# Kernel tuning notes

Hardware: AMD Instinct MI355X
Metric: run time of the kernel (lower is better)

Reference implementation:

```python
import jax, jax.numpy as jnp
import numpy as np
from functools import partial

IMG = 800.0
LEVEL_HW = [13, 25, 50, 100, 200]  # p6..p2 (reverse-sorted dict order)
NUM_A = 3
A_TOTAL = NUM_A * sum(h * h for h in LEVEL_HW)  # 159882


def _rand_boxes(key, shape, img=IMG):
    k1, k2, k3, k4 = jax.random.split(key, 4)
    cx = jax.random.uniform(k1, shape, minval=0.0, maxval=img)
    cy = jax.random.uniform(k2, shape, minval=0.0, maxval=img)
    w = jax.random.uniform(k3, shape, minval=16.0, maxval=256.0)
    h = jax.random.uniform(k4, shape, minval=16.0, maxval=256.0)
    return jnp.stack([cx - w / 2, cy - h / 2, cx + w / 2, cy + h / 2], axis=-1)


def setup_inputs() -> dict:
    key = jax.random.key(0)
    ks = jax.random.split(key, 16)
    feats = {}
    for i, (name, hw) in enumerate(zip(['f_p6', 'f_p5', 'f_p4', 'f_p3', 'f_p2'], LEVEL_HW)):
        feats[name] = jax.random.normal(ks[i], (2, 256, hw, hw), dtype=jnp.float32)
    anchors = _rand_boxes(ks[5], (A_TOTAL,))
    gt_bboxes = _rand_boxes(ks[6], (2, 20))
    w_in = jax.random.normal(ks[7], (256, 256, 3, 3), dtype=jnp.float32) * 0.02
    b_in = jnp.zeros((256,), jnp.float32)
    w_obj = jax.random.normal(ks[8], (3, 256, 1, 1), dtype=jnp.float32) * 0.02
    b_obj = jnp.zeros((3,), jnp.float32)
    w_del = jax.random.normal(ks[9], (12, 256, 1, 1), dtype=jnp.float32) * 0.02
    b_del = jnp.zeros((12,), jnp.float32)
    return dict(**feats, anchors=anchors, gt_bboxes=gt_bboxes,
                w_in=w_in, b_in=b_in, w_obj=w_obj, b_obj=b_obj,
                w_del=w_del, b_del=b_del)


def _conv(x, w, b, pad):
    y = jax.lax.conv_general_dilated(x, w, (1, 1), [(pad, pad), (pad, pad)],
                                     dimension_numbers=('NCHW', 'OIHW', 'NCHW'))
    return y + b[None, :, None, None]


def _pairwise_iou(b1, b2):
    # b1 [A,4], b2 [G,4] -> [A,G]
    a1 = (b1[:, 2] - b1[:, 0]) * (b1[:, 3] - b1[:, 1])
    a2 = (b2[:, 2] - b2[:, 0]) * (b2[:, 3] - b2[:, 1])
    lt = jnp.maximum(b1[:, None, :2], b2[None, :, :2])
    rb = jnp.minimum(b1[:, None, 2:], b2[None, :, 2:])
    wh = jnp.clip(rb - lt, 0.0)
    inter = wh[..., 0] * wh[..., 1]
    return inter / (a1[:, None] + a2[None, :] - inter)


def _get_deltas(src, tgt):
    sw = src[:, 2] - src[:, 0]; sh = src[:, 3] - src[:, 1]
    scx = src[:, 0] + 0.5 * sw; scy = src[:, 1] + 0.5 * sh
    tw = tgt[:, 2] - tgt[:, 0]; th = tgt[:, 3] - tgt[:, 1]
    tcx = tgt[:, 0] + 0.5 * tw; tcy = tgt[:, 1] + 0.5 * th
    return jnp.stack([(tcx - scx) / sw, (tcy - scy) / sh,
                      jnp.log(tw / sw), jnp.log(th / sh)], axis=-1)


def _per_image(logits, deltas, gt, anchors):
    # logits [A], deltas [A,4], gt [G,4]
    iou = _pairwise_iou(anchors, gt)                      # [A,G]
    matched = jnp.argmax(iou, axis=1)                     # [A]
    mval = jnp.max(iou, axis=1)
    label = jnp.where(mval >= 0.7, 1.0, jnp.where(mval < 0.3, 0.0, -1.0))
    # low-quality matches: best anchor per gt is positive
    best_per_gt = jnp.max(iou, axis=0)                    # [G]
    lq = jnp.any((iou == best_per_gt[None, :]) & (best_per_gt[None, :] > 0), axis=1)
    label = jnp.where(lq, 1.0, label)
    # deterministic subsample: up to 128 pos, fill to 256 with neg
    pos_mask = label == 1.0
    neg_mask = label == 0.0
    sel_pos = pos_mask & (jnp.cumsum(pos_mask.astype(jnp.int32)) <= 128)
    n_pos = jnp.sum(sel_pos.astype(jnp.int32))
    sel_neg = neg_mask & (jnp.cumsum(neg_mask.astype(jnp.int32)) <= (256 - n_pos))
    valid = sel_pos | sel_neg
    # BCE with logits, sum over sampled anchors
    tgt = jnp.clip(label, 0.0, 1.0)
    bce = jnp.maximum(logits, 0.0) - logits * tgt + jnp.log1p(jnp.exp(-jnp.abs(logits)))
    obj_loss = jnp.sum(jnp.where(valid, bce, 0.0))
    # smooth-L1 with beta=0 == L1, only on positives
    gt_d = _get_deltas(anchors, gt[matched])              # [A,4]
    l1 = jnp.sum(jnp.abs(deltas - gt_d), axis=-1)
    loc_loss = jnp.sum(jnp.where(sel_pos, l1, 0.0))
    return obj_loss, loc_loss


def _forward(f_p6, f_p5, f_p4, f_p3, f_p2, anchors, gt_bboxes,
             w_in, b_in, w_obj, b_obj, w_del, b_del):
    logits_all, deltas_all = [], []
    for fm in (f_p6, f_p5, f_p4, f_p3, f_p2):  # reverse-sorted fm order
        x = jax.nn.relu(_conv(fm, w_in, b_in, 1))
        lg = _conv(x, w_obj, b_obj, 0)                    # [B,3,H,W]
        dl = _conv(x, w_del, b_del, 0)                    # [B,12,H,W]
        B, _, H, W = lg.shape
        logits_all.append(jnp.transpose(lg, (0, 2, 3, 1)).reshape(B, -1))
        dl = dl.reshape(B, NUM_A, 4, H, W)
        deltas_all.append(jnp.transpose(dl, (0, 3, 4, 1, 2)).reshape(B, -1, 4))
    logits = jnp.concatenate(logits_all, axis=1)          # [B,A]
    deltas = jnp.concatenate(deltas_all, axis=1)          # [B,A,4]
    obj, loc = jax.vmap(_per_image, in_axes=(0, 0, 0, None))(logits, deltas, gt_bboxes, anchors)
    return (obj[0] + obj[1]) / 2.0, (loc[0] + loc[1]) / 2.0


def reference(f_p6, f_p5, f_p4, f_p3, f_p2, anchors, gt_bboxes,
              w_in, b_in, w_obj, b_obj, w_del, b_del):
    return _forward(f_p6, f_p5, f_p4, f_p3, f_p2, anchors, gt_bboxes,
                    w_in, b_in, w_obj, b_obj, w_del, b_del)
```

## Files before the change

kernel.cpp:

```cpp
#include <hip/hip_runtime.h>
#include <hip/hip_bf16.h>
#include <math.h>

#define A_TOTAL 159882
#define NGT 20
#define NBLK 625
#define ANB 4
#define WTBLK 288


__device__ __forceinline__ float iou_one(float ax1, float ay1, float ax2, float ay2,
                                         float gx1, float gy1, float gx2, float gy2) {
    float a1 = (ax2 - ax1) * (ay2 - ay1);
    float a2 = (gx2 - gx1) * (gy2 - gy1);
    float ltx = fmaxf(ax1, gx1), lty = fmaxf(ay1, gy1);
    float rbx = fminf(ax2, gx2), rby = fminf(ay2, gy2);
    float w = fmaxf(rbx - ltx, 0.f), h = fmaxf(rby - lty, 0.f);
    float inter = w * h;
    return inter / (a1 + a2 - inter);
}

__device__ __forceinline__ void decode_anchor(int a, int& W, int& aid, int& y, int& x, int& lvl) {
    int off;
    if      (a < 507)   { off = 0;     W = 13;  lvl = 0; }
    else if (a < 2382)  { off = 507;   W = 25;  lvl = 1; }
    else if (a < 9882)  { off = 2382;  W = 50;  lvl = 2; }
    else if (a < 39882) { off = 9882;  W = 100; lvl = 3; }
    else                { off = 39882; W = 200; lvl = 4; }
    int rel = a - off;
    aid = rel % 3;
    int pos = rel / 3;
    y = pos / W; x = pos % W;
}

__global__ __launch_bounds__(256) void k1_bmax_wtrans(
    const float* __restrict__ anchors, const float* __restrict__ gt,
    const float* __restrict__ w_in,
    float* __restrict__ pmax, float* __restrict__ wt) {
    const int bx = blockIdx.x, img = blockIdx.y;
    const int tid = threadIdx.x;
    if (bx >= NBLK) {
        int idx = ((bx - NBLK) * 2 + img) * 256 + tid;
        int co = idx / 576, k4 = idx - co * 576;
        float4 v = *(const float4*)(w_in + (size_t)co * 2304 + k4 * 4);
        ((float4*)wt)[(size_t)k4 * 256 + co] = v;
        return;
    }
    __shared__ float sgt[NGT * 4];
    __shared__ float sred[4][NGT];
    if (tid < NGT * 4) sgt[tid] = gt[img * NGT * 4 + tid];
    __syncthreads();
    const int a = bx * 256 + tid;
    float4 ab = make_float4(0.f, 0.f, 1.f, 1.f);
    if (a < A_TOTAL) ab = ((const float4*)anchors)[a];
    const int lane = tid & 63, wid = tid >> 6;
    #pragma unroll
    for (int g = 0; g < NGT; g++) {
        float u = (a < A_TOTAL)
                    ? iou_one(ab.x, ab.y, ab.z, ab.w,
                              sgt[g * 4], sgt[g * 4 + 1], sgt[g * 4 + 2], sgt[g * 4 + 3])
                    : 0.f;
        #pragma unroll
        for (int o = 32; o > 0; o >>= 1) u = fmaxf(u, __shfl_down(u, o));
        if (lane == 0) sred[wid][g] = u;
    }
    __syncthreads();
    if (tid < NGT) {
        float u = fmaxf(fmaxf(sred[0][tid], sred[1][tid]),
                        fmaxf(sred[2][tid], sred[3][tid]));
        pmax[((size_t)img * NBLK + bx) * NGT + tid] = u;
    }
}

__global__ __launch_bounds__(256) void k2_label(
    const float* __restrict__ anchors, const float* __restrict__ gt,
    const float* __restrict__ pmax,
    unsigned char* __restrict__ packed, unsigned int* __restrict__ blk_cnt) {
    const int img = blockIdx.y, blk = blockIdx.x;
    const int tid = threadIdx.x;
    const int lane = tid & 63, wid = tid >> 6;
    __shared__ float sgt[NGT * 4];
    __shared__ float sred[4][NGT];
    __shared__ float bestl[NGT];
    __shared__ int wp[4], wn[4];
    if (tid < NGT * 4) sgt[tid] = gt[img * NGT * 4 + tid];

    float bl[NGT];
    #pragma unroll
    for (int g = 0; g < NGT; g++) bl[g] = 0.f;
    for (int i = tid; i < NBLK; i += 256) {
        const float* pr = pmax + ((size_t)img * NBLK + i) * NGT;
        #pragma unroll
        for (int g = 0; g < NGT; g++) bl[g] = fmaxf(bl[g], pr[g]);
    }
    #pragma unroll
    for (int g = 0; g < NGT; g++) {
        float u = bl[g];
        #pragma unroll
        for (int o = 32; o > 0; o >>= 1) u = fmaxf(u, __shfl_down(u, o));
        if (lane == 0) sred[wid][g] = u;
    }
    __syncthreads();
    if (tid < NGT)
        bestl[tid] = fmaxf(fmaxf(sred[0][tid], sred[1][tid]),
                           fmaxf(sred[2][tid], sred[3][tid]));
    __syncthreads();

    const int a = blk * 256 + tid;
    const bool act = a < A_TOTAL;
    int code = 2;
    if (act) {
        float4 ab = ((const float4*)anchors)[a];
        float mval = -1.f; int arg = 0; bool lq = false;
        #pragma unroll
        for (int g = 0; g < NGT; g++) {
            float v = iou_one(ab.x, ab.y, ab.z, ab.w,
                              sgt[g * 4], sgt[g * 4 + 1], sgt[g * 4 + 2], sgt[g * 4 + 3]);
            if (v > mval) { mval = v; arg = g; }
            if (__float_as_uint(v) == __float_as_uint(bestl[g]) && v > 0.f) lq = true;
        }
        if (lq || mval >= 0.7f) code = 1;
        else if (mval < 0.3f)   code = 0;
        packed[(size_t)img * A_TOTAL + a] = (unsigned char)((code << 5) | arg);
    }
    unsigned long long bp = __ballot(act && code == 1);
    unsigned long long bn = __ballot(act && code == 0);
    if (lane == 0) { wp[wid] = __popcll(bp); wn[wid] = __popcll(bn); }
    __syncthreads();
    if (tid == 0) {
        unsigned int p = wp[0] + wp[1] + wp[2] + wp[3];
        unsigned int n = wn[0] + wn[1] + wn[2] + wn[3];
        blk_cnt[img * NBLK + blk] = (p << 16) | n;
    }
}

__global__ __launch_bounds__(256) void k3_select(
    const unsigned char* __restrict__ packed,
    const unsigned int* __restrict__ blk_cnt,
    int* __restrict__ sel, int* __restrict__ sel_count) {
    const int img = blockIdx.y, blk = blockIdx.x;
    const int tid = threadIdx.x;
    const int lane = tid & 63, wid = tid >> 6;
    __shared__ unsigned long long sscan[8];
    __shared__ int wcnt[8];

    unsigned long long tot = 0ULL, pre = 0ULL;
    const int j0 = tid * 3;
    #pragma unroll
    for (int j = 0; j < 3; j++) {
        int i = j0 + j;
        if (i < NBLK) {
            unsigned u = blk_cnt[img * NBLK + i];
            unsigned long long w = ((unsigned long long)(u >> 16) << 32) | (u & 0xFFFFu);
            tot += w;
            if (i < blk) pre += w;
        }
    }
    #pragma unroll
    for (int o = 32; o > 0; o >>= 1) {
        tot += __shfl_down(tot, o);
        pre += __shfl_down(pre, o);
    }
    if (lane == 0) { sscan[wid] = tot; sscan[4 + wid] = pre; }
    __syncthreads();
    unsigned long long tota = sscan[0] + sscan[1] + sscan[2] + sscan[3];
    unsigned long long prea = sscan[4] + sscan[5] + sscan[6] + sscan[7];
    int tp = (int)(tota >> 32), tn = (int)(tota & 0xFFFFFFFFull);
    int npos = min(tp, 128), capn = 256 - npos;
    if (blk == 0 && tid == 0) sel_count[img] = npos + min(tn, capn);
    int base_p = (int)(prea >> 32), base_n = (int)(prea & 0xFFFFFFFFull);

    const int a = blk * 256 + tid;
    const bool act = a < A_TOTAL;
    int code = act ? (packed[(size_t)img * A_TOTAL + a] >> 5) : 2;
    const bool isp = act && code == 1;
    const bool isn = act && code == 0;
    unsigned long long bp = __ballot(isp);
    unsigned long long bn = __ballot(isn);
    if (lane == 0) { wcnt[wid] = __popcll(bp); wcnt[4 + wid] = __popcll(bn); }
    __syncthreads();
    const unsigned long long mlt = (1ULL << lane) - 1ULL;
    int rp = __popcll(bp & mlt), rn = __popcll(bn & mlt);
    for (int w = 0; w < 4; w++)
        if (w < wid) { rp += wcnt[w]; rn += wcnt[4 + w]; }
    if (isp) { int r = base_p + rp; if (r < npos) sel[img * 256 + r] = a | (1 << 30); }
    if (isn) { int r = base_n + rn; if (r < capn) sel[img * 256 + npos + r] = a; }
}

template <int TRM>
__device__ __forceinline__ void stage_patches(
    const float* __restrict__ f0, const float* __restrict__ f1,
    const float* __restrict__ f2, const float* __restrict__ f3,
    const float* __restrict__ f4,
    const int* __restrict__ sel, int nsel, int img, int chunk, int slot0,
    float (&patch)[ANB][TRM],
    int (&s_W)[ANB], int (&s_y)[ANB], int (&s_x)[ANB], int (&s_act)[ANB],
    const float* (&s_fm)[ANB]) {
    constexpr int CIP = TRM / 9;
    const int tid = threadIdx.x;
    if (tid < ANB) {
        int slot = slot0 + tid;
        bool act = slot < nsel;
        int e = act ? sel[img * 256 + slot] : 0;
        int a = e & 0x3FFFFFFF;
        int W, aid, y, x, lvl;
        decode_anchor(a, W, aid, y, x, lvl);
        s_W[tid] = W; s_y[tid] = y; s_x[tid] = x; s_act[tid] = act ? 1 : 0;
        s_fm[tid] = (lvl == 0 ? f0 : lvl == 1 ? f1 : lvl == 2 ? f2 : lvl == 3 ? f3 : f4);
    }
    __syncthreads();
    for (int p = tid; p < ANB * TRM; p += 256) {
        int aa = p / TRM;
        int idx = p - aa * TRM;
        int cil = idx / 9;
        int r = idx - cil * 9;
        int ky = r / 3, kx = r - ky * 3;
        int W = s_W[aa];
        int yy = s_y[aa] + ky - 1, xx = s_x[aa] + kx - 1;
        float v = 0.f;
        if (s_act[aa] && yy >= 0 && yy < W && xx >= 0 && xx < W) {
            const float* fm = s_fm[aa];
            int ci = chunk * CIP + cil;
            v = fm[(((size_t)img * 256 + ci) * W + yy) * W + xx];
        }
        patch[aa][idx] = v;
    }
    __syncthreads();
}

template <int NCH>
__global__ __launch_bounds__(256) void k_convT(
    const float* __restrict__ f0, const float* __restrict__ f1,
    const float* __restrict__ f2, const float* __restrict__ f3,
    const float* __restrict__ f4,
    const float* __restrict__ wt,
    const int* __restrict__ sel, const int* __restrict__ sel_count,
    float* __restrict__ xpart) {
    constexpr int CIP = 256 / NCH;
    constexpr int TRM = CIP * 9;
    const int img = blockIdx.z;
    const int chunk = blockIdx.y;
    const int slot0 = blockIdx.x * ANB;
    const int nsel = sel_count[img];
    if (slot0 >= nsel) return;

    __shared__ __align__(16) float patch[ANB][TRM];
    __shared__ int s_W[ANB], s_y[ANB], s_x[ANB], s_act[ANB];
    __shared__ const float* s_fm[ANB];
    stage_patches<TRM>(f0, f1, f2, f3, f4, sel, nsel, img, chunk, slot0,
                       patch, s_W, s_y, s_x, s_act, s_fm);

    const int c = threadIdx.x;
    const float4* wt4 = (const float4*)wt + (size_t)(chunk * (TRM / 4)) * 256 + c;
    const float4* p0 = (const float4*)patch[0];
    const float4* p1 = (const float4*)patch[1];
    const float4* p2 = (const float4*)patch[2];
    const float4* p3 = (const float4*)patch[3];
    float acc0 = 0.f, acc1 = 0.f, acc2 = 0.f, acc3 = 0.f;
    #pragma unroll 8
    for (int i = 0; i < TRM / 4; i++) {
        float4 w = wt4[(size_t)i * 256];
        float4 q;
        q = p0[i]; acc0 += w.x * q.x + w.y * q.y + w.z * q.z + w.w * q.w;
        q = p1[i]; acc1 += w.x * q.x + w.y * q.y + w.z * q.z + w.w * q.w;
        q = p2[i]; acc2 += w.x * q.x + w.y * q.y + w.z * q.z + w.w * q.w;
        q = p3[i]; acc3 += w.x * q.x + w.y * q.y + w.z * q.z + w.w * q.w;
    }
    float acc[ANB] = {acc0, acc1, acc2, acc3};
    #pragma unroll
    for (int aa = 0; aa < ANB; aa++) {
        int slot = slot0 + aa;
        if (slot < nsel)
            xpart[(((size_t)img * NCH + chunk) * 256 + slot) * 256 + c] = acc[aa];
    }
}

template <int NCH>
__global__ __launch_bounds__(256) void k_post(
    const float* __restrict__ xpart,
    const float* __restrict__ anchors, const float* __restrict__ gt,
    const float* __restrict__ b_in,
    const float* __restrict__ w_obj, const float* __restrict__ b_obj,
    const float* __restrict__ w_del, const float* __restrict__ b_del,
    const unsigned char* __restrict__ packed,
    const int* __restrict__ sel, const int* __restrict__ sel_count,
    float* __restrict__ lossbuf) {
    const int img = blockIdx.y;
    const int slot = blockIdx.x;
    const int nsel = sel_count[img];
    if (slot >= nsel) return;
    const int e = sel[img * 256 + slot];
    const int is_pos = (e >> 30) & 1;
    const int a = e & 0x3FFFFFFF;
    int W, aid, y, x, lvl;
    decode_anchor(a, W, aid, y, x, lvl);

    const int c = threadIdx.x;
    float s = b_in[c];
    #pragma unroll
    for (int ch = 0; ch < NCH; ch++)
        s += xpart[(((size_t)img * NCH + ch) * 256 + slot) * 256 + c];
    float xf = fmaxf(s, 0.f);

    float part[5];
    part[0] = xf * w_obj[aid * 256 + c];
    #pragma unroll
    for (int j = 0; j < 4; j++) part[1 + j] = xf * w_del[(aid * 4 + j) * 256 + c];
    const int lane = c & 63, wid = c >> 6;
    __shared__ float red[5][4];
    #pragma unroll
    for (int o = 32; o > 0; o >>= 1)
        #pragma unroll
        for (int j = 0; j < 5; j++) part[j] += __shfl_down(part[j], o);
    if (lane == 0)
        #pragma unroll
        for (int j = 0; j < 5; j++) red[j][wid] = part[j];
    __syncthreads();

    if (c == 0) {
        float logit = red[0][0] + red[0][1] + red[0][2] + red[0][3] + b_obj[aid];
        float tgt = is_pos ? 1.f : 0.f;
        float bce = fmaxf(logit, 0.f) - logit * tgt + log1pf(expf(-fabsf(logit)));
        float l1 = 0.f;
        if (is_pos) {
            float d[4];
            #pragma unroll
            for (int j = 0; j < 4; j++)
                d[j] = red[1 + j][0] + red[1 + j][1] + red[1 + j][2] + red[1 + j][3] + b_del[aid * 4 + j];
            int m = packed[(size_t)img * A_TOTAL + a] & 31;
            const float* sp = anchors + (size_t)a * 4;
            const float* t = gt + (size_t)(img * NGT + m) * 4;
            float sw = sp[2] - sp[0], sh = sp[3] - sp[1];
            float scx = sp[0] + 0.5f * sw, scy = sp[1] + 0.5f * sh;
            float tw = t[2] - t[0], th = t[3] - t[1];
            float tcx = t[0] + 0.5f * tw, tcy = t[1] + 0.5f * th;
            float g0 = (tcx - scx) / sw, g1 = (tcy - scy) / sh;
            float g2 = logf(tw / sw),    g3 = logf(th / sh);
            l1 = fabsf(d[0] - g0) + fabsf(d[1] - g1) + fabsf(d[2] - g2) + fabsf(d[3] - g3);
        }
        lossbuf[(img * 256 + slot) * 2 + 0] = bce;
        lossbuf[(img * 256 + slot) * 2 + 1] = l1;
    }
}

__global__ void k_final(const float* __restrict__ lossbuf,
                        const int* __restrict__ sel_count,
                        float* __restrict__ out) {
    const int t = threadIdx.x;
    const int img = t >> 8, slot = t & 255;
    float bce = 0.f, l1 = 0.f;
    if (slot < sel_count[img]) {
        bce = lossbuf[t * 2 + 0];
        l1  = lossbuf[t * 2 + 1];
    }
    const int lane = t & 63, wid = t >> 6;
    #pragma unroll
    for (int o = 32; o > 0; o >>= 1) {
        bce += __shfl_down(bce, o);
        l1  += __shfl_down(l1, o);
    }
    __shared__ float rb[8], rl[8];
    if (lane == 0) { rb[wid] = bce; rl[wid] = l1; }
    __syncthreads();
    if (t == 0) {
        float sb = 0.f, sl = 0.f;
        #pragma unroll
        for (int w = 0; w < 8; w++) { sb += rb[w]; sl += rl[w]; }
        out[0] = 0.5f * sb;
        out[1] = 0.5f * sl;
    }
}

__global__ void k_init(unsigned int* best, float* out) {
    int t = threadIdx.x;
    if (t < 2 * NGT) best[t] = 0u;
    if (t < 2) out[t] = 0.f;
}

__global__ void k_best(const float* __restrict__ anchors, const float* __restrict__ gt,
                       unsigned int* best) {
    const int img = blockIdx.y;
    __shared__ float sgt[NGT * 4];
    __shared__ float sred[4][NGT];
    const int tid = threadIdx.x;
    if (tid < NGT * 4) sgt[tid] = gt[img * NGT * 4 + tid];
    __syncthreads();
    float vmax[NGT];
    #pragma unroll
    for (int g = 0; g < NGT; g++) vmax[g] = 0.f;
    const int stride = gridDim.x * blockDim.x;
    for (int a = blockIdx.x * blockDim.x + tid; a < A_TOTAL; a += stride) {
        float4 ab = ((const float4*)anchors)[a];
        #pragma unroll
        for (int g = 0; g < NGT; g++) {
            float v = iou_one(ab.x, ab.y, ab.z, ab.w,
                              sgt[g * 4], sgt[g * 4 + 1], sgt[g * 4 + 2], sgt[g * 4 + 3]);
            vmax[g] = fmaxf(vmax[g], v);
        }
    }
    const int lane = tid & 63, wid = tid >> 6;
    #pragma unroll
    for (int g = 0; g < NGT; g++) {
        float v = vmax[g];
        #pragma unroll
        for (int o = 32; o > 0; o >>= 1) v = fmaxf(v, __shfl_down(v, o));
        if (lane == 0) sred[wid][g] = v;
    }
    __syncthreads();
    if (tid < NGT) {
        float v = fmaxf(fmaxf(sred[0][tid], sred[1][tid]),
                        fmaxf(sred[2][tid], sred[3][tid]));
        atomicMax(&best[img * NGT + tid], __float_as_uint(v));
    }
}

__global__ void k_label_old(const float* __restrict__ anchors, const float* __restrict__ gt,
                            const unsigned int* __restrict__ best,
                            unsigned char* packed, unsigned int* blk_cnt) {
    const int img = blockIdx.y;
    __shared__ float sgt[NGT * 4];
    __shared__ unsigned int sbest[NGT];
    __shared__ int wp[4], wn[4];
    const int tid = threadIdx.x;
    if (tid < NGT * 4) sgt[tid] = gt[img * NGT * 4 + tid];
    if (tid < NGT) sbest[tid] = best[img * NGT + tid];
    __syncthreads();
    const int a = blockIdx.x * blockDim.x + tid;
    const bool act = a < A_TOTAL;
    int code = 2;
    if (act) {
        float4 ab = ((const float4*)anchors)[a];
        float mval = -1.f; int arg = 0; bool lq = false;
        #pragma unroll
        for (int g = 0; g < NGT; g++) {
            float v = iou_one(ab.x, ab.y, ab.z, ab.w,
                              sgt[g * 4], sgt[g * 4 + 1], sgt[g * 4 + 2], sgt[g * 4 + 3]);
            if (v > mval) { mval = v; arg = g; }
            if (__float_as_uint(v) == sbest[g] && v > 0.f) lq = true;
        }
        if (lq || mval >= 0.7f) code = 1;
        else if (mval < 0.3f)   code = 0;
        packed[(size_t)img * A_TOTAL + a] = (unsigned char)((code << 5) | arg);
    }
    unsigned long long bp = __ballot(act && code == 1);
    unsigned long long bn = __ballot(act && code == 0);
    const int lane = tid & 63, wid = tid >> 6;
    if (lane == 0) { wp[wid] = __popcll(bp); wn[wid] = __popcll(bn); }
    __syncthreads();
    if (tid == 0) {
        unsigned int p = wp[0] + wp[1] + wp[2] + wp[3];
        unsigned int n = wn[0] + wn[1] + wn[2] + wn[3];
        blk_cnt[img * NBLK + blockIdx.x] = (p << 16) | n;
    }
}

__global__ __launch_bounds__(256) void k_eval(
    const float* __restrict__ f0, const float* __restrict__ f1,
    const float* __restrict__ f2, const float* __restrict__ f3,
    const float* __restrict__ f4,
    const float* __restrict__ anchors, const float* __restrict__ gt,
    const float* __restrict__ w_in, const float* __restrict__ b_in,
    const float* __restrict__ w_obj, const float* __restrict__ b_obj,
    const float* __restrict__ w_del, const float* __restrict__ b_del,
    const unsigned char* __restrict__ packed,
    const int* __restrict__ sel, const int* __restrict__ sel_count,
    float* out) {
    const int img = blockIdx.x >> 6;
    const int slot0 = (blockIdx.x & 63) * 4;
    const int nsel = sel_count[img];
    if (slot0 >= nsel) return;

    __shared__ __align__(16) float patch[4][2304];
    __shared__ float red[4][5][4];
    __shared__ float lsum[2];
    const int c = threadIdx.x;
    if (c < 2) lsum[c] = 0.f;

    bool actv[4]; int av[4], aidv[4], isposv[4];
    #pragma unroll
    for (int aa = 0; aa < 4; aa++) {
        int slot = slot0 + aa;
        bool act = slot < nsel;
        actv[aa] = act;
        int e = act ? sel[img * 256 + slot] : 0;
        isposv[aa] = (e >> 30) & 1;
        int a = e & 0x3FFFFFFF;
        av[aa] = a;
        int W, aid, y, x, lvl;
        decode_anchor(a, W, aid, y, x, lvl);
        aidv[aa] = aid;
        const float* fm = lvl == 0 ? f0 : lvl == 1 ? f1 : lvl == 2 ? f2 : lvl == 3 ? f3 : f4;
        const float* ch = fm + ((size_t)img * 256 + c) * W * W;
        #pragma unroll
        for (int ky = 0; ky < 3; ky++)
            #pragma unroll
            for (int kx = 0; kx < 3; kx++) {
                int yy = y + ky - 1, xx = x + kx - 1;
                float v = (act && yy >= 0 && yy < W && xx >= 0 && xx < W) ? ch[yy * W + xx] : 0.f;
                patch[aa][c * 9 + ky * 3 + kx] = v;
            }
    }
    __syncthreads();

    const float bi = b_in[c];
    float acc0 = bi, acc1 = bi, acc2 = bi, acc3 = bi;
    const float4* wr = (const float4*)(w_in + (size_t)c * 2304);
    const float4* p0 = (const float4*)patch[0];
    const float4* p1 = (const float4*)patch[1];
    const float4* p2 = (const float4*)patch[2];
    const float4* p3 = (const float4*)patch[3];
    #pragma unroll 4
    for (int i = 0; i < 576; i++) {
        float4 w = wr[i];
        float4 q;
        q = p0[i]; acc0 += w.x * q.x + w.y * q.y + w.z * q.z + w.w * q.w;
        q = p1[i]; acc1 += w.x * q.x + w.y * q.y + w.z * q.z + w.w * q.w;
        q = p2[i]; acc2 += w.x * q.x + w.y * q.y + w.z * q.z + w.w * q.w;
        q = p3[i]; acc3 += w.x * q.x + w.y * q.y + w.z * q.z + w.w * q.w;
    }
    float xf[4] = { fmaxf(acc0, 0.f), fmaxf(acc1, 0.f), fmaxf(acc2, 0.f), fmaxf(acc3, 0.f) };

    float part[4][5];
    #pragma unroll
    for (int aa = 0; aa < 4; aa++) {
        part[aa][0] = xf[aa] * w_obj[aidv[aa] * 256 + c];
        #pragma unroll
        for (int j = 0; j < 4; j++)
            part[aa][1 + j] = xf[aa] * w_del[(aidv[aa] * 4 + j) * 256 + c];
    }
    const int lane = c & 63, wid = c >> 6;
    #pragma unroll
    for (int o = 32; o > 0; o >>= 1)
        #pragma unroll
        for (int aa = 0; aa < 4; aa++)
            #pragma unroll
            for (int j = 0; j < 5; j++)
                part[aa][j] += __shfl_down(part[aa][j], o);
    if (lane == 0)
        #pragma unroll
        for (int aa = 0; aa < 4; aa++)
            #pragma unroll
            for (int j = 0; j < 5; j++)
                red[aa][j][wid] = part[aa][j];
    __syncthreads();

    if (c < 4 && actv[c]) {
        const int aa = c;
        float logit = red[aa][0][0] + red[aa][0][1] + red[aa][0][2] + red[aa][0][3] + b_obj[aidv[aa]];
        float tgt = isposv[aa] ? 1.f : 0.f;
        float bce = fmaxf(logit, 0.f) - logit * tgt + log1pf(expf(-fabsf(logit)));
        atomicAdd(&lsum[0], bce);
        if (isposv[aa]) {
            float d[4];
            #pragma unroll
            for (int j = 0; j < 4; j++)
                d[j] = red[aa][1 + j][0] + red[aa][1 + j][1] + red[aa][1 + j][2] + red[aa][1 + j][3]
                       + b_del[aidv[aa] * 4 + j];
            int a = av[aa];
            int m = packed[(size_t)img * A_TOTAL + a] & 31;
            const float* s = anchors + (size_t)a * 4;
            const float* t = gt + (size_t)(img * NGT + m) * 4;
            float sw = s[2] - s[0], sh = s[3] - s[1];
            float scx = s[0] + 0.5f * sw, scy = s[1] + 0.5f * sh;
            float tw = t[2] - t[0], th = t[3] - t[1];
            float tcx = t[0] + 0.5f * tw, tcy = t[1] + 0.5f * th;
            float g0 = (tcx - scx) / sw, g1 = (tcy - scy) / sh;
            float g2 = logf(tw / sw),    g3 = logf(th / sh);
            float l1 = fabsf(d[0] - g0) + fabsf(d[1] - g1) + fabsf(d[2] - g2) + fabsf(d[3] - g3);
            atomicAdd(&lsum[1], l1);
        }
    }
    __syncthreads();
    if (c == 0) {
        atomicAdd(&out[0], 0.5f * lsum[0]);
        atomicAdd(&out[1], 0.5f * lsum[1]);
    }
}

extern "C" void kernel_launch(void* const* d_in, const int* in_sizes, int n_in,
                              void* d_out, int out_size, void* d_ws, size_t ws_size,
                              hipStream_t stream) {
    const float* f_p6 = (const float*)d_in[0];
    const float* f_p5 = (const float*)d_in[1];
    const float* f_p4 = (const float*)d_in[2];
    const float* f_p3 = (const float*)d_in[3];
    const float* f_p2 = (const float*)d_in[4];
    const float* anchors = (const float*)d_in[5];
    const float* gt      = (const float*)d_in[6];
    const float* w_in  = (const float*)d_in[7];
    const float* b_in  = (const float*)d_in[8];
    const float* w_obj = (const float*)d_in[9];
    const float* b_obj = (const float*)d_in[10];
    const float* w_del = (const float*)d_in[11];
    const float* b_del = (const float*)d_in[12];
    float* out = (float*)d_out;
    char* ws = (char*)d_ws;

    unsigned int* best    = (unsigned int*)(ws + 0);
    int* sel_count        = (int*)(ws + 168);
    int* sel              = (int*)(ws + 192);
    unsigned int* blk_cnt = (unsigned int*)(ws + 2240);
    unsigned char* packed = (unsigned char*)(ws + 17344);
    float* lossbuf        = (float*)(ws + 337152);
    float* xpart          = (float*)(ws + 341248);
    float* pmax           = (float*)(ws + 341248);
    float* wt             = (float*)(ws + 341248 + 4194304);
    const size_t WS_NEED = 341248 + 4194304 + 2359296;

    if (ws_size >= WS_NEED) {
        k1_bmax_wtrans<<<dim3(NBLK + WTBLK, 2), 256, 0, stream>>>(anchors, gt, w_in, pmax, wt);
        k2_label<<<dim3(NBLK, 2), 256, 0, stream>>>(anchors, gt, pmax, packed, blk_cnt);
        k3_select<<<dim3(NBLK, 2), 256, 0, stream>>>(packed, blk_cnt, sel, sel_count);
        k_convT<8><<<dim3(64, 8, 2), 256, 0, stream>>>(f_p6, f_p5, f_p4, f_p3, f_p2,
                                                       wt, sel, sel_count, xpart);
        k_post<8><<<dim3(256, 2), 256, 0, stream>>>(xpart, anchors, gt, b_in,
                                                    w_obj, b_obj, w_del, b_del,
                                                    packed, sel, sel_count, lossbuf);
        k_final<<<1, 512, 0, stream>>>(lossbuf, sel_count, out);
    } else {
        k_init<<<1, 64, 0, stream>>>(best, out);
        k_best<<<dim3(64, 2), 256, 0, stream>>>(anchors, gt, best);
        k_label_old<<<dim3(NBLK, 2), 256, 0, stream>>>(anchors, gt, best, packed, blk_cnt);
        k3_select<<<dim3(NBLK, 2), 256, 0, stream>>>(packed, blk_cnt, sel, sel_count);
        k_eval<<<128, 256, 0, stream>>>(f_p6, f_p5, f_p4, f_p3, f_p2,
                                        anchors, gt, w_in, b_in, w_obj, b_obj,
                                        w_del, b_del, packed, sel, sel_count, out);
    }
}
```

Baseline: 69.10 us.

## Cache per-anchor IoU max/mask in k1 and retile selected-anchor conv

The first kernel now stores each anchor's max IoU, argmax and a bitmask of GTs where its IoU equals the block-local max. A small reduction kernel then builds the global per-GT best, so the labeling kernel no longer recomputes 20 IoUs per anchor or re-reduces pmax in every block. The sparse 3x3 conv over selected anchors changes from 4 anchors × 8 channel chunks to 8 anchors × 16 chunks, which doubles weight reuse per block and adds more partial sums for the post kernel to combine. The trade-offs are an extra launch, about 2.5MB of extra per-anchor writes and reads, and a larger xpart buffer.

```diff
diff --git a/kernel.cpp b/kernel.cpp
--- a/kernel.cpp
+++ b/kernel.cpp
@@ -5,7 +5,6 @@
 #define A_TOTAL 159882
 #define NGT 20
 #define NBLK 625
-#define ANB 4
 #define WTBLK 288
 
 
@@ -36,7 +35,8 @@
 __global__ __launch_bounds__(256) void k1_bmax_wtrans(
     const float* __restrict__ anchors, const float* __restrict__ gt,
     const float* __restrict__ w_in,
-    float* __restrict__ pmax, float* __restrict__ wt) {
+    float* __restrict__ pmax, float* __restrict__ mv, unsigned* __restrict__ aux,
+    float* __restrict__ wt) {
     const int bx = blockIdx.x, img = blockIdx.y;
     const int tid = threadIdx.x;
     if (bx >= NBLK) {
@@ -48,18 +48,26 @@
     }
     __shared__ float sgt[NGT * 4];
     __shared__ float sred[4][NGT];
+    __shared__ float pblk[NGT];
     if (tid < NGT * 4) sgt[tid] = gt[img * NGT * 4 + tid];
     __syncthreads();
     const int a = bx * 256 + tid;
+    const bool act = a < A_TOTAL;
     float4 ab = make_float4(0.f, 0.f, 1.f, 1.f);
-    if (a < A_TOTAL) ab = ((const float4*)anchors)[a];
+    if (act) ab = ((const float4*)anchors)[a];
     const int lane = tid & 63, wid = tid >> 6;
+    float v[NGT];
+    float mval = -1.f; int arg = 0;
     #pragma unroll
     for (int g = 0; g < NGT; g++) {
-        float u = (a < A_TOTAL)
-                    ? iou_one(ab.x, ab.y, ab.z, ab.w,
-                              sgt[g * 4], sgt[g * 4 + 1], sgt[g * 4 + 2], sgt[g * 4 + 3])
-                    : 0.f;
+        float u = act ? iou_one(ab.x, ab.y, ab.z, ab.w,
+                                sgt[g*4], sgt[g*4+1], sgt[g*4+2], sgt[g*4+3]) : 0.f;
+        v[g] = u;
+        if (u > mval) { mval = u; arg = g; }
+    }
+    #pragma unroll
+    for (int g = 0; g < NGT; g++) {
+        float u = v[g];
         #pragma unroll
         for (int o = 32; o > 0; o >>= 1) u = fmaxf(u, __shfl_down(u, o));
         if (lane == 0) sred[wid][g] = u;
@@ -68,60 +76,64 @@
     if (tid < NGT) {
         float u = fmaxf(fmaxf(sred[0][tid], sred[1][tid]),
                         fmaxf(sred[2][tid], sred[3][tid]));
+        pblk[tid] = u;
         pmax[((size_t)img * NBLK + bx) * NGT + tid] = u;
     }
+    __syncthreads();
+    if (act) {
+        unsigned mask = 0;
+        #pragma unroll
+        for (int g = 0; g < NGT; g++)
+            if (v[g] == pblk[g] && v[g] > 0.f) mask |= (1u << g);
+        mv[(size_t)img * A_TOTAL + a] = mval;
+        aux[(size_t)img * A_TOTAL + a] = (mask << 5) | (unsigned)arg;
+    }
+}
+
+__global__ void k_bred(const float* __restrict__ pmax, unsigned int* __restrict__ best) {
+    const int g = blockIdx.x, img = blockIdx.y;
+    const int tid = threadIdx.x;
+    float v = 0.f;
+    for (int i = tid; i < NBLK; i += 256)
+        v = fmaxf(v, pmax[((size_t)img * NBLK + i) * NGT + g]);
+    const int lane = tid & 63, wid = tid >> 6;
+    #pragma unroll
+    for (int o = 32; o > 0; o >>= 1) v = fmaxf(v, __shfl_down(v, o));
+    __shared__ float r[4];
+    if (lane == 0) r[wid] = v;
+    __syncthreads();
+    if (tid == 0)
+        best[img * NGT + g] = __float_as_uint(fmaxf(fmaxf(r[0], r[1]), fmaxf(r[2], r[3])));
 }
 
 __global__ __launch_bounds__(256) void k2_label(
-    const float* __restrict__ anchors, const float* __restrict__ gt,
-    const float* __restrict__ pmax,
+    const float* __restrict__ mv, const unsigned* __restrict__ aux,
+    const float* __restrict__ pmax, const unsigned int* __restrict__ best,
     unsigned char* __restrict__ packed, unsigned int* __restrict__ blk_cnt) {
     const int img = blockIdx.y, blk = blockIdx.x;
     const int tid = threadIdx.x;
     const int lane = tid & 63, wid = tid >> 6;
-    __shared__ float sgt[NGT * 4];
-    __shared__ float sred[4][NGT];
-    __shared__ float bestl[NGT];
+    __shared__ float sbest[NGT], pblk[NGT];
     __shared__ int wp[4], wn[4];
-    if (tid < NGT * 4) sgt[tid] = gt[img * NGT * 4 + tid];
-
-    float bl[NGT];
-    #pragma unroll
-    for (int g = 0; g < NGT; g++) bl[g] = 0.f;
-    for (int i = tid; i < NBLK; i += 256) {
-        const float* pr = pmax + ((size_t)img * NBLK + i) * NGT;
-        #pragma unroll
-        for (int g = 0; g < NGT; g++) bl[g] = fmaxf(bl[g], pr[g]);
-    }
-    #pragma unroll
-    for (int g = 0; g < NGT; g++) {
-        float u = bl[g];
-        #pragma unroll
-        for (int o = 32; o > 0; o >>= 1) u = fmaxf(u, __shfl_down(u, o));
-        if (lane == 0) sred[wid][g] = u;
-    }
-    __syncthreads();
-    if (tid < NGT)
-        bestl[tid] = fmaxf(fmaxf(sred[0][tid], sred[1][tid]),
-                           fmaxf(sred[2][tid], sred[3][tid]));
-    __syncthreads();
-
+    if (tid < NGT) {
+        sbest[tid] = __uint_as_float(best[img * NGT + tid]);
+        pblk[tid]  = pmax[((size_t)img * NBLK + blk) * NGT + tid];
+    }
+    __syncthreads();
     const int a = blk * 256 + tid;
     const bool act = a < A_TOTAL;
     int code = 2;
     if (act) {
-        float4 ab = ((const float4*)anchors)[a];
-        float mval = -1.f; int arg = 0; bool lq = false;
-        #pragma unroll
-        for (int g = 0; g < NGT; g++) {
-            float v = iou_one(ab.x, ab.y, ab.z, ab.w,
-                              sgt[g * 4], sgt[g * 4 + 1], sgt[g * 4 + 2], sgt[g * 4 + 3]);
-            if (v > mval) { mval = v; arg = g; }
-            if (__float_as_uint(v) == __float_as_uint(bestl[g]) && v > 0.f) lq = true;
-        }
+        float mval = mv[(size_t)img * A_TOTAL + a];
+        unsigned ax = aux[(size_t)img * A_TOTAL + a];
+        unsigned mask = ax >> 5;
+        bool lq = false;
+        #pragma unroll
+        for (int g = 0; g < NGT; g++)
+            if (((mask >> g) & 1u) && (pblk[g] == sbest[g])) lq = true;
         if (lq || mval >= 0.7f) code = 1;
         else if (mval < 0.3f)   code = 0;
-        packed[(size_t)img * A_TOTAL + a] = (unsigned char)((code << 5) | arg);
+        packed[(size_t)img * A_TOTAL + a] = (unsigned char)((code << 5) | (ax & 31u));
     }
     unsigned long long bp = __ballot(act && code == 1);
     unsigned long long bn = __ballot(act && code == 0);
@@ -187,96 +199,74 @@
     if (isn) { int r = base_n + rn; if (r < capn) sel[img * 256 + npos + r] = a; }
 }
 
-template <int TRM>
-__device__ __forceinline__ void stage_patches(
+__global__ __launch_bounds__(256) void k_convT16(
     const float* __restrict__ f0, const float* __restrict__ f1,
     const float* __restrict__ f2, const float* __restrict__ f3,
     const float* __restrict__ f4,
-    const int* __restrict__ sel, int nsel, int img, int chunk, int slot0,
-    float (&patch)[ANB][TRM],
-    int (&s_W)[ANB], int (&s_y)[ANB], int (&s_x)[ANB], int (&s_act)[ANB],
-    const float* (&s_fm)[ANB]) {
-    constexpr int CIP = TRM / 9;
+    const float* __restrict__ wt,
+    const int* __restrict__ sel, const int* __restrict__ sel_count,
+    float* __restrict__ xpart) {
+    const int img = blockIdx.z;
+    const int chunk = blockIdx.y;
+    const int slot0 = blockIdx.x * 8;
+    const int nsel = sel_count[img];
+    if (slot0 >= nsel) return;
+
+    __shared__ __align__(16) float patch[8][144];
+    __shared__ int sW[8], sY[8], sX[8], sAct[8];
+    __shared__ const float* sfm[8];
     const int tid = threadIdx.x;
-    if (tid < ANB) {
+
+    if (tid < 8) {
         int slot = slot0 + tid;
         bool act = slot < nsel;
         int e = act ? sel[img * 256 + slot] : 0;
         int a = e & 0x3FFFFFFF;
         int W, aid, y, x, lvl;
         decode_anchor(a, W, aid, y, x, lvl);
-        s_W[tid] = W; s_y[tid] = y; s_x[tid] = x; s_act[tid] = act ? 1 : 0;
-        s_fm[tid] = (lvl == 0 ? f0 : lvl == 1 ? f1 : lvl == 2 ? f2 : lvl == 3 ? f3 : f4);
-    }
-    __syncthreads();
-    for (int p = tid; p < ANB * TRM; p += 256) {
-        int aa = p / TRM;
-        int idx = p - aa * TRM;
+        sW[tid] = W; sY[tid] = y; sX[tid] = x; sAct[tid] = act ? 1 : 0;
+        sfm[tid] = (lvl == 0 ? f0 : lvl == 1 ? f1 : lvl == 2 ? f2 : lvl == 3 ? f3 : f4);
+    }
+    __syncthreads();
+
+    for (int p = tid; p < 8 * 144; p += 256) {
+        int aa = p / 144;
+        int idx = p - aa * 144;
         int cil = idx / 9;
         int r = idx - cil * 9;
         int ky = r / 3, kx = r - ky * 3;
-        int W = s_W[aa];
-        int yy = s_y[aa] + ky - 1, xx = s_x[aa] + kx - 1;
+        int W = sW[aa];
+        int yy = sY[aa] + ky - 1, xx = sX[aa] + kx - 1;
         float v = 0.f;
-        if (s_act[aa] && yy >= 0 && yy < W && xx >= 0 && xx < W) {
-            const float* fm = s_fm[aa];
-            int ci = chunk * CIP + cil;
-            v = fm[(((size_t)img * 256 + ci) * W + yy) * W + xx];
+        if (sAct[aa] && yy >= 0 && yy < W && xx >= 0 && xx < W) {
+            int ci = chunk * 16 + cil;
+            v = sfm[aa][(((size_t)img * 256 + ci) * W + yy) * W + xx];
         }
         patch[aa][idx] = v;
     }
     __syncthreads();
-}
-
-template <int NCH>
-__global__ __launch_bounds__(256) void k_convT(
-    const float* __restrict__ f0, const float* __restrict__ f1,
-    const float* __restrict__ f2, const float* __restrict__ f3,
-    const float* __restrict__ f4,
-    const float* __restrict__ wt,
-    const int* __restrict__ sel, const int* __restrict__ sel_count,
-    float* __restrict__ xpart) {
-    constexpr int CIP = 256 / NCH;
-    constexpr int TRM = CIP * 9;
-    const int img = blockIdx.z;
-    const int chunk = blockIdx.y;
-    const int slot0 = blockIdx.x * ANB;
-    const int nsel = sel_count[img];
-    if (slot0 >= nsel) return;
-
-    __shared__ __align__(16) float patch[ANB][TRM];
-    __shared__ int s_W[ANB], s_y[ANB], s_x[ANB], s_act[ANB];
-    __shared__ const float* s_fm[ANB];
-    stage_patches<TRM>(f0, f1, f2, f3, f4, sel, nsel, img, chunk, slot0,
-                       patch, s_W, s_y, s_x, s_act, s_fm);
-
-    const int c = threadIdx.x;
-    const float4* wt4 = (const float4*)wt + (size_t)(chunk * (TRM / 4)) * 256 + c;
-    const float4* p0 = (const float4*)patch[0];
-    const float4* p1 = (const float4*)patch[1];
-    const float4* p2 = (const float4*)patch[2];
-    const float4* p3 = (const float4*)patch[3];
-    float acc0 = 0.f, acc1 = 0.f, acc2 = 0.f, acc3 = 0.f;
-    #pragma unroll 8
-    for (int i = 0; i < TRM / 4; i++) {
+
+    const int c = tid;
+    const float4* wt4 = (const float4*)wt + (size_t)(chunk * 36) * 256 + c;
+    float acc[8] = {0.f, 0.f, 0.f, 0.f, 0.f, 0.f, 0.f, 0.f};
+    #pragma unroll 4
+    for (int i = 0; i < 36; i++) {
         float4 w = wt4[(size_t)i * 256];
-        float4 q;
-        q = p0[i]; acc0 += w.x * q.x + w.y * q.y + w.z * q.z + w.w * q.w;
-        q = p1[i]; acc1 += w.x * q.x + w.y * q.y + w.z * q.z + w.w * q.w;
-        q = p2[i]; acc2 += w.x * q.x + w.y * q.y + w.z * q.z + w.w * q.w;
-        q = p3[i]; acc3 += w.x * q.x + w.y * q.y + w.z * q.z + w.w * q.w;
-    }
-    float acc[ANB] = {acc0, acc1, acc2, acc3};
-    #pragma unroll
-    for (int aa = 0; aa < ANB; aa++) {
+        #pragma unroll
+        for (int aa = 0; aa < 8; aa++) {
+            float4 q = ((const float4*)patch[aa])[i];
+            acc[aa] += w.x * q.x + w.y * q.y + w.z * q.z + w.w * q.w;
+        }
+    }
+    #pragma unroll
+    for (int aa = 0; aa < 8; aa++) {
         int slot = slot0 + aa;
         if (slot < nsel)
-            xpart[(((size_t)img * NCH + chunk) * 256 + slot) * 256 + c] = acc[aa];
-    }
-}
-
-template <int NCH>
-__global__ __launch_bounds__(256) void k_post(
+            xpart[(((size_t)img * 16 + chunk) * 256 + slot) * 256 + c] = acc[aa];
+    }
+}
+
+__global__ __launch_bounds__(256) void k_post16(
     const float* __restrict__ xpart,
     const float* __restrict__ anchors, const float* __restrict__ gt,
     const float* __restrict__ b_in,
@@ -298,8 +288,8 @@
     const int c = threadIdx.x;
     float s = b_in[c];
     #pragma unroll
-    for (int ch = 0; ch < NCH; ch++)
-        s += xpart[(((size_t)img * NCH + ch) * 256 + slot) * 256 + c];
+    for (int ch = 0; ch < 16; ch++)
+        s += xpart[(((size_t)img * 16 + ch) * 256 + slot) * 256 + c];
     float xf = fmaxf(s, 0.f);
 
     float part[5];
@@ -602,20 +592,24 @@
     unsigned int* blk_cnt = (unsigned int*)(ws + 2240);
     unsigned char* packed = (unsigned char*)(ws + 17344);
     float* lossbuf        = (float*)(ws + 337152);
-    float* xpart          = (float*)(ws + 341248);
-    float* pmax           = (float*)(ws + 341248);
-    float* wt             = (float*)(ws + 341248 + 4194304);
-    const size_t WS_NEED = 341248 + 4194304 + 2359296;
+    float* mv             = (float*)(ws + 341248);
+    unsigned* aux         = (unsigned*)(ws + 1620352);
+    float* pmax           = (float*)(ws + 2899456);
+    float* xpart          = (float*)(ws + 2999552);
+    float* wt             = (float*)(ws + 11388160);
+    const size_t WS_NEED  = 13747456;
 
     if (ws_size >= WS_NEED) {
-        k1_bmax_wtrans<<<dim3(NBLK + WTBLK, 2), 256, 0, stream>>>(anchors, gt, w_in, pmax, wt);
-        k2_label<<<dim3(NBLK, 2), 256, 0, stream>>>(anchors, gt, pmax, packed, blk_cnt);
+        k1_bmax_wtrans<<<dim3(NBLK + WTBLK, 2), 256, 0, stream>>>(anchors, gt, w_in,
+                                                                  pmax, mv, aux, wt);
+        k_bred<<<dim3(NGT, 2), 256, 0, stream>>>(pmax, best);
+        k2_label<<<dim3(NBLK, 2), 256, 0, stream>>>(mv, aux, pmax, best, packed, blk_cnt);
         k3_select<<<dim3(NBLK, 2), 256, 0, stream>>>(packed, blk_cnt, sel, sel_count);
-        k_convT<8><<<dim3(64, 8, 2), 256, 0, stream>>>(f_p6, f_p5, f_p4, f_p3, f_p2,
+        k_convT16<<<dim3(32, 16, 2), 256, 0, stream>>>(f_p6, f_p5, f_p4, f_p3, f_p2,
                                                        wt, sel, sel_count, xpart);
-        k_post<8><<<dim3(256, 2), 256, 0, stream>>>(xpart, anchors, gt, b_in,
-                                                    w_obj, b_obj, w_del, b_del,
-                                                    packed, sel, sel_count, lossbuf);
+        k_post16<<<dim3(256, 2), 256, 0, stream>>>(xpart, anchors, gt, b_in,
+                                                   w_obj, b_obj, w_del, b_del,
+                                                   packed, sel, sel_count, lossbuf);
         k_final<<<1, 512, 0, stream>>>(lossbuf, sel_count, out);
     } else {
         k_init<<<1, 64, 0, stream>>>(best, out);
```

Measured after the change: 63.16 us, median of 2. 1.09x faster.
